# Performance work log

Hardware: AMD Instinct MI355X
Metric: run time of the kernel (lower is better)

Reference implementation:

```python
import jax, jax.numpy as jnp
import numpy as np
from jax import lax

R_WIN = 1
WIN = 2 * R_WIN + 1        # 3
K = WIN * WIN              # 9
STRIDE = 4
LATENT = 128
N_LVL = 2


def _conv_relu(x, w, b):
    # x: (B*S, 3, H, W), w: (128, 3, 7, 7) -> (B*S, 128, H/4, W/4)
    y = lax.conv_general_dilated(x, w, (STRIDE, STRIDE), [(3, 3), (3, 3)],
                                 dimension_numbers=('NCHW', 'OIHW', 'NCHW'))
    return jax.nn.relu(y + b[None, :, None, None])


def _bilinear_sample(fmap, gx, gy):
    # fmap (B,C,H,W); gx,gy (B,P) in [-1,1]; align_corners=True, zeros padding
    B, C, H, W = fmap.shape
    ix = (gx + 1.0) * 0.5 * (W - 1)
    iy = (gy + 1.0) * 0.5 * (H - 1)
    x0 = jnp.floor(ix); y0 = jnp.floor(iy)
    x1 = x0 + 1.0;      y1 = y0 + 1.0
    wx1 = ix - x0; wx0 = 1.0 - wx1
    wy1 = iy - y0; wy0 = 1.0 - wy1

    fm_flat = fmap.reshape(B, C, H * W)

    def corner(xf, yf, wgt):
        valid = (xf >= 0) & (xf <= W - 1) & (yf >= 0) & (yf <= H - 1)
        xi = jnp.clip(xf, 0, W - 1).astype(jnp.int32)
        yi = jnp.clip(yf, 0, H - 1).astype(jnp.int32)
        idx = yi * W + xi                              # (B,P)
        g = jax.vmap(lambda fm, ii: fm[:, ii])(fm_flat, idx)  # (B,C,P)
        return g * (wgt * valid)[:, None, :]

    return (corner(x0, y0, wx0 * wy0) + corner(x1, y0, wx1 * wy0)
            + corner(x0, y1, wx0 * wy1) + corner(x1, y1, wx1 * wy1))


def _sample_features(fmap, pts):
    B, C, H, W = fmap.shape
    N = pts.shape[1]
    lin = jnp.linspace(-R_WIN, R_WIN, WIN)
    dy, dx = jnp.meshgrid(lin, lin, indexing='ij')
    off = jnp.stack([dx / (W - 1) * 2.0, dy / (H - 1) * 2.0], -1).reshape(-1, 2)  # (K,2)
    grid = (pts * 2.0 - 1.0)[:, :, None, :] + off[None, None]   # (B,N,K,2)
    grid = grid.reshape(B, N * K, 2)
    s = _bilinear_sample(fmap, grid[..., 0], grid[..., 1])       # (B,C,N*K)
    return s.reshape(B, C, N, WIN, WIN)


def _l2norm(x, axis):
    return x / jnp.maximum(jnp.linalg.norm(x, axis=axis, keepdims=True), 1e-12)


def _forward(queries, frames, conv_w, conv_b, w1, b1, wp, bp, wv, bv):
    B, S, C, H, W = frames.shape
    N = queries.shape[1]
    x = 2.0 * (frames / 255.0) - 1.0
    fm = _conv_relu(x.reshape(B * S, C, H, W), conv_w, conv_b)
    fm = fm.reshape(B, S, LATENT, H // STRIDE, W // STRIDE)

    pyr = [fm]
    for _ in range(N_LVL - 1):
        fm = lax.reduce_window(fm, 0.0, lax.add, (1, 1, 1, WIN, WIN),
                               (1, 1, 1, WIN, WIN), 'VALID') / float(WIN * WIN)
        pyr.append(fm)

    cur = queries                                   # pred_pos aliases queries in torch
    vis_acc = jnp.zeros((B, N), queries.dtype)
    for i in range(N_LVL):
        f5 = pyr[N_LVL - 1 - i]                     # (B,S,C,h,w) coarse -> fine
        feats = _sample_features(f5[:, 0], cur).reshape(B, LATENT, N, K)
        matches = _sample_features(f5[:, 1], cur).reshape(B, LATENT, N, K)
        fn = _l2norm(feats, 1)
        mn = _l2norm(matches, 1)
        corr = jnp.einsum('bcnh,bcnk->bnhk', fn, mn).reshape(B * N, K * K)
        h = jax.nn.relu(corr @ w1 + b1)
        pred = jax.nn.softmax(h @ wp + bp, axis=-1).reshape(B, N, WIN, WIN)
        vis = jax.nn.sigmoid(h @ wv + bv).reshape(B, N)
        hh, ww = f5.shape[3], f5.shape[4]
        dsx = jnp.linspace(-R_WIN / (ww - 1), R_WIN / (ww - 1), WIN)
        dsy = jnp.linspace(-R_WIN / (hh - 1), R_WIN / (hh - 1), WIN)
        d_x = pred.sum(-1) @ dsx                    # (B,N)
        d_y = pred.sum(-2) @ dsy                    # (B,N)
        cur = jnp.stack([cur[..., 0] + d_x, cur[..., 1] + d_y], -1)
        vis_acc = vis_acc + vis
    return cur, vis_acc / float(N_LVL)


def setup_inputs() -> dict:
    key = jax.random.key(0)
    ks = jax.random.split(key, 8)
    B, S, N, H, W = 2, 2, 8192, 384, 512
    return {
        'queries': jax.random.uniform(ks[0], (B, N, 2), jnp.float32),
        'frames': jax.random.uniform(ks[1], (B, S, 3, H, W), jnp.float32) * 255.0,
        'conv_w': jax.random.normal(ks[2], (128, 3, 7, 7), jnp.float32) * 0.02,
        'conv_b': jnp.zeros((128,), jnp.float32),
        'w1': jax.random.normal(ks[3], (81, 256), jnp.float32) * 0.05,
        'b1': jnp.zeros((256,), jnp.float32),
        'wp': jax.random.normal(ks[4], (256, 9), jnp.float32) * 0.05,
        'bp': jnp.zeros((9,), jnp.float32),
        'wv': jax.random.normal(ks[5], (256, 1), jnp.float32) * 0.05,
        'bv': jnp.zeros((1,), jnp.float32),
    }


def reference(queries, frames, conv_w, conv_b, w1, b1, wp, bp, wv, bv):
    return _forward(queries, frames, conv_w, conv_b, w1, b1, wp, bp, wv, bv)
```

## Files before the change

### kernel.cpp

```cpp
#include <hip/hip_runtime.h>
#include <math.h>

#define NQ 8192
#define NP 16384
#define H_IN 384
#define W_IN 512
#define HH0 96
#define WW0 128
#define HH1 32
#define WW1 42

__global__ void transpose_w_kernel(const float* __restrict__ w, float* __restrict__ wT) {
    int idx = blockIdx.x * 256 + threadIdx.x;
    if (idx < 147 * 128) {
        int tap = idx >> 7;
        int oc  = idx & 127;
        wT[idx] = w[oc * 147 + tap];
    }
}

__global__ __launch_bounds__(256) void conv_kernel(
    const float* __restrict__ frames, const float* __restrict__ wT,
    const float* __restrict__ bias, float* __restrict__ out)
{
    __shared__ float lds[3 * 7 * 136];
    const int bs  = blockIdx.z;
    const int oh  = blockIdx.y;
    const int ow0 = blockIdx.x * 32;
    const int tid = threadIdx.x;

    for (int idx = tid; idx < 3 * 7 * 134; idx += 256) {
        int c   = idx / 938;
        int rem = idx - c * 938;
        int kh  = rem / 134;
        int col = rem - kh * 134;
        int gy  = oh * 4 - 3 + kh;
        int gx  = ow0 * 4 - 3 + col;
        float v = 0.0f;
        if (gy >= 0 && gy < H_IN && gx >= 0 && gx < W_IN) {
            float t = frames[((size_t)(bs * 3 + c) * H_IN + gy) * W_IN + gx];
            v = 2.0f * (t / 255.0f) - 1.0f;
        }
        lds[(c * 7 + kh) * 136 + col] = v;
    }
    __syncthreads();

    const int oc = tid & 63;
    const int g  = tid >> 6;
    float a0[8], a1[8];
#pragma unroll
    for (int p = 0; p < 8; ++p) { a0[p] = 0.0f; a1[p] = 0.0f; }

#pragma unroll
    for (int c = 0; c < 3; ++c) {
#pragma unroll
        for (int kh = 0; kh < 7; ++kh) {
            const float* row = lds + (c * 7 + kh) * 136 + g * 32;
            float4 r4[9];
#pragma unroll
            for (int j = 0; j < 9; ++j) r4[j] = *(const float4*)(row + j * 4);
            float w0[7], w1v[7];
#pragma unroll
            for (int kw = 0; kw < 7; ++kw) {
                int tap = (c * 7 + kh) * 7 + kw;
                w0[kw]  = wT[tap * 128 + oc];
                w1v[kw] = wT[tap * 128 + oc + 64];
            }
#pragma unroll
            for (int p = 0; p < 8; ++p) {
                const float4 A  = r4[p];
                const float4 Bv = r4[p + 1];
                float s0 = a0[p], s1 = a1[p];
                s0 = fmaf(A.x,  w0[0], s0);  s1 = fmaf(A.x,  w1v[0], s1);
                s0 = fmaf(A.y,  w0[1], s0);  s1 = fmaf(A.y,  w1v[1], s1);
                s0 = fmaf(A.z,  w0[2], s0);  s1 = fmaf(A.z,  w1v[2], s1);
                s0 = fmaf(A.w,  w0[3], s0);  s1 = fmaf(A.w,  w1v[3], s1);
                s0 = fmaf(Bv.x, w0[4], s0);  s1 = fmaf(Bv.x, w1v[4], s1);
                s0 = fmaf(Bv.y, w0[5], s0);  s1 = fmaf(Bv.y, w1v[5], s1);
                s0 = fmaf(Bv.z, w0[6], s0);  s1 = fmaf(Bv.z, w1v[6], s1);
                a0[p] = s0; a1[p] = s1;
            }
        }
    }

    const float b0  = bias[oc];
    const float b1b = bias[oc + 64];
#pragma unroll
    for (int p = 0; p < 8; ++p) {
        int ow = ow0 + g * 8 + p;
        size_t ob = ((size_t)(bs * HH0 + oh) * WW0 + ow) * 128;
        out[ob + oc]      = fmaxf(a0[p] + b0, 0.0f);
        out[ob + oc + 64] = fmaxf(a1[p] + b1b, 0.0f);
    }
}

__global__ void pool_kernel(const float* __restrict__ in, float* __restrict__ out) {
    int idx = blockIdx.x * 256 + threadIdx.x;
    if (idx >= 4 * HH1 * WW1 * 128) return;
    int c = idx & 127;
    int r = idx >> 7;
    int px = r % WW1; r /= WW1;
    int py = r % HH1;
    int bs = r / HH1;
    float s = 0.0f;
#pragma unroll
    for (int dy = 0; dy < 3; ++dy)
#pragma unroll
        for (int dx = 0; dx < 3; ++dx)
            s += in[(((size_t)bs * HH0 + py * 3 + dy) * WW0 + px * 3 + dx) * 128 + c];
    out[idx] = s / 9.0f;
}

__global__ __launch_bounds__(512) void sample_kernel(
    const float* __restrict__ fm, int hh, int ww,
    const float* __restrict__ cur_in, float* __restrict__ corr_out)
{
    __shared__ float smem[4 * 2400];
    const int tid  = threadIdx.x;
    const int wvi  = tid >> 6;
    const int lane = tid & 63;
    const int ps   = wvi >> 1;
    const int mp   = wvi & 1;
    const int p    = blockIdx.x * 4 + ps;
    const int b    = p >> 13;

    float* fl    = smem + ps * 2400;
    float* ml    = fl + 1188;
    float* inv_s = fl + 2376;

    const float2 pxy = *(const float2*)(cur_in + (size_t)p * 2);
    const float wwm1 = (float)(ww - 1);
    const float hhm1 = (float)(hh - 1);
    const float ix = ((pxy.x * 2.0f - 1.0f) + 1.0f) * 0.5f * wwm1;
    const float iy = ((pxy.y * 2.0f - 1.0f) + 1.0f) * 0.5f * hhm1;
    const float x0 = floorf(ix), y0 = floorf(iy);
    const float fx1 = ix - x0, fx0 = 1.0f - fx1;
    const float fy1 = iy - y0, fy0 = 1.0f - fy1;

    int   cx[4], cy[4];
    float vx[4], vy[4];
#pragma unroll
    for (int j = 0; j < 4; ++j) {
        float xc = x0 + (float)(j - 1);
        vx[j] = (xc >= 0.0f && xc <= wwm1) ? 1.0f : 0.0f;
        cx[j] = (int)fminf(fmaxf(xc, 0.0f), wwm1);
        float yc = y0 + (float)(j - 1);
        vy[j] = (yc >= 0.0f && yc <= hhm1) ? 1.0f : 0.0f;
        cy[j] = (int)fminf(fmaxf(yc, 0.0f), hhm1);
    }
    float cwx[6], cwy[6];
#pragma unroll
    for (int t = 0; t < 3; ++t) {
        cwx[t * 2 + 0] = fx0 * vx[t]; cwx[t * 2 + 1] = fx1 * vx[t + 1];
        cwy[t * 2 + 0] = fy0 * vy[t]; cwy[t * 2 + 1] = fy1 * vy[t + 1];
    }

    {
        const float2* src = (const float2*)fm + (size_t)(b * 2 + mp) * hh * ww * 64;
        float* dst = mp ? ml : fl;
        float2 P[4][4];
#pragma unroll
        for (int j = 0; j < 4; ++j)
#pragma unroll
            for (int i = 0; i < 4; ++i)
                P[j][i] = src[(cy[j] * ww + cx[i]) * 64 + lane];
#pragma unroll
        for (int ky = 0; ky < 3; ++ky)
#pragma unroll
            for (int kx = 0; kx < 3; ++kx) {
                float wA = cwy[ky * 2 + 0] * cwx[kx * 2 + 0];
                float wB = cwy[ky * 2 + 0] * cwx[kx * 2 + 1];
                float wC = cwy[ky * 2 + 1] * cwx[kx * 2 + 0];
                float wD = cwy[ky * 2 + 1] * cwx[kx * 2 + 1];
                float sx = wA * P[ky][kx].x;
                sx = fmaf(wB, P[ky][kx + 1].x, sx);
                sx = fmaf(wC, P[ky + 1][kx].x, sx);
                sx = fmaf(wD, P[ky + 1][kx + 1].x, sx);
                float sy = wA * P[ky][kx].y;
                sy = fmaf(wB, P[ky][kx + 1].y, sy);
                sy = fmaf(wC, P[ky + 1][kx].y, sy);
                sy = fmaf(wD, P[ky + 1][kx + 1].y, sy);
                *(float2*)(dst + (ky * 3 + kx) * 132 + 2 * lane) = make_float2(sx, sy);
            }
    }
    __syncthreads();

    const int e = mp * 64 + lane;
    float s = 0.0f;
    {
        const float *rA, *rB;
        if (e < 81)      { rA = fl + (e / 9) * 132; rB = ml + (e % 9) * 132; }
        else if (e < 90) { rA = fl + (e - 81) * 132; rB = rA; }
        else             { int em = e - 90; if (em > 8) em = 8;
                           rA = ml + em * 132; rB = rA; }
#pragma unroll
        for (int c = 0; c < 128; c += 4) {
            float4 a  = *(const float4*)(rA + c);
            float4 bb = *(const float4*)(rB + c);
            s += a.x * bb.x; s += a.y * bb.y; s += a.z * bb.z; s += a.w * bb.w;
        }
    }
    if (e >= 81 && e < 90)      inv_s[e - 81]     = 1.0f / fmaxf(sqrtf(s), 1e-12f);
    else if (e >= 90 && e < 99) inv_s[e - 90 + 9] = 1.0f / fmaxf(sqrtf(s), 1e-12f);
    __syncthreads();

    if (e < 81)
        corr_out[(size_t)p * 81 + e] = s * inv_s[e / 9] * inv_s[9 + e % 9];
}

__global__ __launch_bounds__(256) void mlp_kernel(
    const float* __restrict__ corr, const float* __restrict__ cur_in,
    const float* __restrict__ w1, const float* __restrict__ b1,
    const float* __restrict__ wp, const float* __restrict__ bp,
    const float* __restrict__ wvw, const float* __restrict__ bvv,
    int hh, int ww,
    float* __restrict__ cur_out,
    const float* __restrict__ vis_in, float* __restrict__ vis_out,
    int is_last)
{
    __shared__ float cls_t[81 * 18];
    __shared__ float wps[256 * 9];
    __shared__ float wvs[256];
    const int tid   = threadIdx.x;
    const int jg    = tid & 31;
    const int pg    = tid >> 5;
    const int pbase = blockIdx.x * 16;

    for (int idx = tid; idx < 16 * 81; idx += 256) {
        int pt = idx / 81, i = idx - pt * 81;
        cls_t[i * 18 + pt] = corr[(size_t)pbase * 81 + idx];
    }
    for (int idx = tid; idx < 2304; idx += 256) wps[idx] = wp[idx];
    wvs[tid] = wvw[tid];
    __syncthreads();

    float h0[8], h1[8];
    {
        const float4* bp4 = (const float4*)(b1 + jg * 8);
        float4 ba = bp4[0], bb = bp4[1];
        h0[0] = ba.x; h0[1] = ba.y; h0[2] = ba.z; h0[3] = ba.w;
        h0[4] = bb.x; h0[5] = bb.y; h0[6] = bb.z; h0[7] = bb.w;
#pragma unroll
        for (int j = 0; j < 8; ++j) h1[j] = h0[j];
    }

    const float* wbase = w1 + jg * 8;
    const float* cvbase = cls_t + pg * 2;
    for (int i = 0; i < 81; i += 3) {
        const float4 a0 = *(const float4*)(wbase + (i    ) * 256);
        const float4 a1 = *(const float4*)(wbase + (i    ) * 256 + 4);
        const float4 b0 = *(const float4*)(wbase + (i + 1) * 256);
        const float4 b1q = *(const float4*)(wbase + (i + 1) * 256 + 4);
        const float4 c0 = *(const float4*)(wbase + (i + 2) * 256);
        const float4 c1 = *(const float4*)(wbase + (i + 2) * 256 + 4);
        const float2 cvA = *(const float2*)(cvbase + (i    ) * 18);
        const float2 cvB = *(const float2*)(cvbase + (i + 1) * 18);
        const float2 cvC = *(const float2*)(cvbase + (i + 2) * 18);
        h0[0] = fmaf(cvA.x, a0.x, h0[0]); h1[0] = fmaf(cvA.y, a0.x, h1[0]);
        h0[1] = fmaf(cvA.x, a0.y, h0[1]); h1[1] = fmaf(cvA.y, a0.y, h1[1]);
        h0[2] = fmaf(cvA.x, a0.z, h0[2]); h1[2] = fmaf(cvA.y, a0.z, h1[2]);
        h0[3] = fmaf(cvA.x, a0.w, h0[3]); h1[3] = fmaf(cvA.y, a0.w, h1[3]);
        h0[4] = fmaf(cvA.x, a1.x, h0[4]); h1[4] = fmaf(cvA.y, a1.x, h1[4]);
        h0[5] = fmaf(cvA.x, a1.y, h0[5]); h1[5] = fmaf(cvA.y, a1.y, h1[5]);
        h0[6] = fmaf(cvA.x, a1.z, h0[6]); h1[6] = fmaf(cvA.y, a1.z, h1[6]);
        h0[7] = fmaf(cvA.x, a1.w, h0[7]); h1[7] = fmaf(cvA.y, a1.w, h1[7]);
        h0[0] = fmaf(cvB.x, b0.x, h0[0]); h1[0] = fmaf(cvB.y, b0.x, h1[0]);
        h0[1] = fmaf(cvB.x, b0.y, h0[1]); h1[1] = fmaf(cvB.y, b0.y, h1[1]);
        h0[2] = fmaf(cvB.x, b0.z, h0[2]); h1[2] = fmaf(cvB.y, b0.z, h1[2]);
        h0[3] = fmaf(cvB.x, b0.w, h0[3]); h1[3] = fmaf(cvB.y, b0.w, h1[3]);
        h0[4] = fmaf(cvB.x, b1q.x, h0[4]); h1[4] = fmaf(cvB.y, b1q.x, h1[4]);
        h0[5] = fmaf(cvB.x, b1q.y, h0[5]); h1[5] = fmaf(cvB.y, b1q.y, h1[5]);
        h0[6] = fmaf(cvB.x, b1q.z, h0[6]); h1[6] = fmaf(cvB.y, b1q.z, h1[6]);
        h0[7] = fmaf(cvB.x, b1q.w, h0[7]); h1[7] = fmaf(cvB.y, b1q.w, h1[7]);
        h0[0] = fmaf(cvC.x, c0.x, h0[0]); h1[0] = fmaf(cvC.y, c0.x, h1[0]);
        h0[1] = fmaf(cvC.x, c0.y, h0[1]); h1[1] = fmaf(cvC.y, c0.y, h1[1]);
        h0[2] = fmaf(cvC.x, c0.z, h0[2]); h1[2] = fmaf(cvC.y, c0.z, h1[2]);
        h0[3] = fmaf(cvC.x, c0.w, h0[3]); h1[3] = fmaf(cvC.y, c0.w, h1[3]);
        h0[4] = fmaf(cvC.x, c1.x, h0[4]); h1[4] = fmaf(cvC.y, c1.x, h1[4]);
        h0[5] = fmaf(cvC.x, c1.y, h0[5]); h1[5] = fmaf(cvC.y, c1.y, h1[5]);
        h0[6] = fmaf(cvC.x, c1.z, h0[6]); h1[6] = fmaf(cvC.y, c1.z, h1[6]);
        h0[7] = fmaf(cvC.x, c1.w, h0[7]); h1[7] = fmaf(cvC.y, c1.w, h1[7]);
    }

    float pl0[10], pl1[10];
#pragma unroll
    for (int o = 0; o < 10; ++o) { pl0[o] = 0.0f; pl1[o] = 0.0f; }
#pragma unroll
    for (int j = 0; j < 8; ++j) {
        const float hv0 = fmaxf(h0[j], 0.0f);
        const float hv1 = fmaxf(h1[j], 0.0f);
        const float* wr = wps + (jg * 8 + j) * 9;
#pragma unroll
        for (int o = 0; o < 9; ++o) {
            const float wv = wr[o];
            pl0[o] = fmaf(hv0, wv, pl0[o]);
            pl1[o] = fmaf(hv1, wv, pl1[o]);
        }
        const float wvv = wvs[jg * 8 + j];
        pl0[9] = fmaf(hv0, wvv, pl0[9]);
        pl1[9] = fmaf(hv1, wvv, pl1[9]);
    }
#pragma unroll
    for (int o = 0; o < 10; ++o) {
        pl0[o] += __shfl_xor(pl0[o], 1);  pl1[o] += __shfl_xor(pl1[o], 1);
        pl0[o] += __shfl_xor(pl0[o], 2);  pl1[o] += __shfl_xor(pl1[o], 2);
        pl0[o] += __shfl_xor(pl0[o], 4);  pl1[o] += __shfl_xor(pl1[o], 4);
        pl0[o] += __shfl_xor(pl0[o], 8);  pl1[o] += __shfl_xor(pl1[o], 8);
        pl0[o] += __shfl_xor(pl0[o], 16); pl1[o] += __shfl_xor(pl1[o], 16);
    }

    if (jg == 0) {
        const float wwm1 = (float)(ww - 1);
        const float hhm1 = (float)(hh - 1);
        const float ax = 1.0f / wwm1;
        const float ay = 1.0f / hhm1;
#pragma unroll
        for (int t = 0; t < 2; ++t) {
            const float* fo = t ? pl1 : pl0;
            const int p = pbase + pg * 2 + t;
            float lg[9];
#pragma unroll
            for (int o = 0; o < 9; ++o) lg[o] = fo[o] + bp[o];
            float mx = lg[0];
#pragma unroll
            for (int o = 1; o < 9; ++o) mx = fmaxf(mx, lg[o]);
            float ex[9], sum = 0.0f;
#pragma unroll
            for (int o = 0; o < 9; ++o) { ex[o] = expf(lg[o] - mx); sum += ex[o]; }
#pragma unroll
            for (int o = 0; o < 9; ++o) ex[o] = ex[o] / sum;

            const float vis = 1.0f / (1.0f + expf(-(fo[9] + bvv[0])));

            const float r0 = ex[0] + ex[1] + ex[2];
            const float r2 = ex[6] + ex[7] + ex[8];
            const float c0 = ex[0] + ex[3] + ex[6];
            const float c2 = ex[2] + ex[5] + ex[8];
            const float dx = r0 * (-ax) + r2 * ax;
            const float dy = c0 * (-ay) + c2 * ay;

            const float2 pq = *(const float2*)(cur_in + (size_t)p * 2);
            *(float2*)(cur_out + (size_t)p * 2) = make_float2(pq.x + dx, pq.y + dy);
            vis_out[p] = is_last ? (vis_in[p] + vis) * 0.5f : vis;
        }
    }
}

extern "C" void kernel_launch(void* const* d_in, const int* in_sizes, int n_in,
                              void* d_out, int out_size, void* d_ws, size_t ws_size,
                              hipStream_t stream) {
    (void)in_sizes; (void)n_in; (void)out_size; (void)ws_size;
    const float* queries = (const float*)d_in[0];
    const float* frames  = (const float*)d_in[1];
    const float* conv_w  = (const float*)d_in[2];
    const float* conv_b  = (const float*)d_in[3];
    const float* w1      = (const float*)d_in[4];
    const float* b1      = (const float*)d_in[5];
    const float* wp      = (const float*)d_in[6];
    const float* bp      = (const float*)d_in[7];
    const float* wvw     = (const float*)d_in[8];
    const float* bvv     = (const float*)d_in[9];
    float* out = (float*)d_out;

    float* ws     = (float*)d_ws;
    float* fm0    = ws;
    float* fm1    = fm0 + 6291456;
    float* wT     = fm1 + 688128;
    float* cur_ws = wT + 18816;
    float* vis_ws = cur_ws + 32768;
    float* corrws = vis_ws + 16384;

    transpose_w_kernel<<<74, 256, 0, stream>>>(conv_w, wT);
    conv_kernel<<<dim3(4, HH0, 4), 256, 0, stream>>>(frames, wT, conv_b, fm0);
    pool_kernel<<<2688, 256, 0, stream>>>(fm0, fm1);

    sample_kernel<<<4096, 512, 0, stream>>>(fm1, HH1, WW1, queries, corrws);
    mlp_kernel<<<1024, 256, 0, stream>>>(corrws, queries, w1, b1, wp, bp, wvw, bvv,
                                         HH1, WW1, cur_ws, nullptr, vis_ws, 0);
    sample_kernel<<<4096, 512, 0, stream>>>(fm0, HH0, WW0, cur_ws, corrws);
    mlp_kernel<<<1024, 256, 0, stream>>>(corrws, cur_ws, w1, b1, wp, bp, wvw, bvv,
                                         HH0, WW0, out, vis_ws, out + 32768, 1);
}
```

Before: 247.0 us.

## Stage MLP weights in LDS and process 64 points per block

The MLP kernel now copies the full 81x256 first-layer weight matrix into shared memory and processes 64 points per 512-thread block, with each thread computing 4 points instead of 2. This reuses each weight load across more points and replaces repeated global weight reads with LDS reads. In exchange it uses about 111KB of LDS per block, which limits occupancy, and launches only 256 blocks. The conv kernel also gets a launch-bounds occupancy hint of 4 blocks per multiprocessor, which may increase register pressure or spilling.

Result: faster. 231.7 us (-6.2%).

```diff
diff --git a/kernel.cpp b/kernel.cpp
--- a/kernel.cpp
+++ b/kernel.cpp
@@ -19,7 +19,7 @@
     }
 }
 
-__global__ __launch_bounds__(256) void conv_kernel(
+__global__ __launch_bounds__(256, 4) void conv_kernel(
     const float* __restrict__ frames, const float* __restrict__ wT,
     const float* __restrict__ bias, float* __restrict__ out)
 {
@@ -208,7 +208,7 @@
         corr_out[(size_t)p * 81 + e] = s * inv_s[e / 9] * inv_s[9 + e % 9];
 }
 
-__global__ __launch_bounds__(256) void mlp_kernel(
+__global__ __launch_bounds__(512) void mlp_kernel(
     const float* __restrict__ corr, const float* __restrict__ cur_in,
     const float* __restrict__ w1, const float* __restrict__ b1,
     const float* __restrict__ wp, const float* __restrict__ bp,
@@ -218,96 +218,86 @@
     const float* __restrict__ vis_in, float* __restrict__ vis_out,
     int is_last)
 {
-    __shared__ float cls_t[81 * 18];
-    __shared__ float wps[256 * 9];
-    __shared__ float wvs[256];
+    __shared__ float w1L[81 * 256];
+    __shared__ float corrL[81 * 68];
+    __shared__ float wpL[256 * 9];
+    __shared__ float wvL[256];
+    __shared__ float b1L[256];
     const int tid   = threadIdx.x;
     const int jg    = tid & 31;
     const int pg    = tid >> 5;
-    const int pbase = blockIdx.x * 16;
-
-    for (int idx = tid; idx < 16 * 81; idx += 256) {
+    const int j0    = jg * 8;
+    const int pbase = blockIdx.x * 64;
+
+    {
+        const float4* src = (const float4*)w1;
+        float4*       dst = (float4*)w1L;
+        for (int idx = tid; idx < 5184; idx += 512) dst[idx] = src[idx];
+    }
+    for (int idx = tid; idx < 64 * 81; idx += 512) {
         int pt = idx / 81, i = idx - pt * 81;
-        cls_t[i * 18 + pt] = corr[(size_t)pbase * 81 + idx];
-    }
-    for (int idx = tid; idx < 2304; idx += 256) wps[idx] = wp[idx];
-    wvs[tid] = wvw[tid];
+        corrL[i * 68 + pt] = corr[(size_t)pbase * 81 + idx];
+    }
+    for (int idx = tid; idx < 2304; idx += 512) wpL[idx] = wp[idx];
+    if (tid < 256) { wvL[tid] = wvw[tid]; b1L[tid] = b1[tid]; }
     __syncthreads();
 
-    float h0[8], h1[8];
-    {
-        const float4* bp4 = (const float4*)(b1 + jg * 8);
-        float4 ba = bp4[0], bb = bp4[1];
-        h0[0] = ba.x; h0[1] = ba.y; h0[2] = ba.z; h0[3] = ba.w;
-        h0[4] = bb.x; h0[5] = bb.y; h0[6] = bb.z; h0[7] = bb.w;
-#pragma unroll
-        for (int j = 0; j < 8; ++j) h1[j] = h0[j];
-    }
-
-    const float* wbase = w1 + jg * 8;
-    const float* cvbase = cls_t + pg * 2;
-    for (int i = 0; i < 81; i += 3) {
-        const float4 a0 = *(const float4*)(wbase + (i    ) * 256);
-        const float4 a1 = *(const float4*)(wbase + (i    ) * 256 + 4);
-        const float4 b0 = *(const float4*)(wbase + (i + 1) * 256);
-        const float4 b1q = *(const float4*)(wbase + (i + 1) * 256 + 4);
-        const float4 c0 = *(const float4*)(wbase + (i + 2) * 256);
-        const float4 c1 = *(const float4*)(wbase + (i + 2) * 256 + 4);
-        const float2 cvA = *(const float2*)(cvbase + (i    ) * 18);
-        const float2 cvB = *(const float2*)(cvbase + (i + 1) * 18);
-        const float2 cvC = *(const float2*)(cvbase + (i + 2) * 18);
-        h0[0] = fmaf(cvA.x, a0.x, h0[0]); h1[0] = fmaf(cvA.y, a0.x, h1[0]);
-        h0[1] = fmaf(cvA.x, a0.y, h0[1]); h1[1] = fmaf(cvA.y, a0.y, h1[1]);
-        h0[2] = fmaf(cvA.x, a0.z, h0[2]); h1[2] = fmaf(cvA.y, a0.z, h1[2]);
-        h0[3] = fmaf(cvA.x, a0.w, h0[3]); h1[3] = fmaf(cvA.y, a0.w, h1[3]);
-        h0[4] = fmaf(cvA.x, a1.x, h0[4]); h1[4] = fmaf(cvA.y, a1.x, h1[4]);
-        h0[5] = fmaf(cvA.x, a1.y, h0[5]); h1[5] = fmaf(cvA.y, a1.y, h1[5]);
-        h0[6] = fmaf(cvA.x, a1.z, h0[6]); h1[6] = fmaf(cvA.y, a1.z, h1[6]);
-        h0[7] = fmaf(cvA.x, a1.w, h0[7]); h1[7] = fmaf(cvA.y, a1.w, h1[7]);
-        h0[0] = fmaf(cvB.x, b0.x, h0[0]); h1[0] = fmaf(cvB.y, b0.x, h1[0]);
-        h0[1] = fmaf(cvB.x, b0.y, h0[1]); h1[1] = fmaf(cvB.y, b0.y, h1[1]);
-        h0[2] = fmaf(cvB.x, b0.z, h0[2]); h1[2] = fmaf(cvB.y, b0.z, h1[2]);
-        h0[3] = fmaf(cvB.x, b0.w, h0[3]); h1[3] = fmaf(cvB.y, b0.w, h1[3]);
-        h0[4] = fmaf(cvB.x, b1q.x, h0[4]); h1[4] = fmaf(cvB.y, b1q.x, h1[4]);
-        h0[5] = fmaf(cvB.x, b1q.y, h0[5]); h1[5] = fmaf(cvB.y, b1q.y, h1[5]);
-        h0[6] = fmaf(cvB.x, b1q.z, h0[6]); h1[6] = fmaf(cvB.y, b1q.z, h1[6]);
-        h0[7] = fmaf(cvB.x, b1q.w, h0[7]); h1[7] = fmaf(cvB.y, b1q.w, h1[7]);
-        h0[0] = fmaf(cvC.x, c0.x, h0[0]); h1[0] = fmaf(cvC.y, c0.x, h1[0]);
-        h0[1] = fmaf(cvC.x, c0.y, h0[1]); h1[1] = fmaf(cvC.y, c0.y, h1[1]);
-        h0[2] = fmaf(cvC.x, c0.z, h0[2]); h1[2] = fmaf(cvC.y, c0.z, h1[2]);
-        h0[3] = fmaf(cvC.x, c0.w, h0[3]); h1[3] = fmaf(cvC.y, c0.w, h1[3]);
-        h0[4] = fmaf(cvC.x, c1.x, h0[4]); h1[4] = fmaf(cvC.y, c1.x, h1[4]);
-        h0[5] = fmaf(cvC.x, c1.y, h0[5]); h1[5] = fmaf(cvC.y, c1.y, h1[5]);
-        h0[6] = fmaf(cvC.x, c1.z, h0[6]); h1[6] = fmaf(cvC.y, c1.z, h1[6]);
-        h0[7] = fmaf(cvC.x, c1.w, h0[7]); h1[7] = fmaf(cvC.y, c1.w, h1[7]);
-    }
-
-    float pl0[10], pl1[10];
-#pragma unroll
-    for (int o = 0; o < 10; ++o) { pl0[o] = 0.0f; pl1[o] = 0.0f; }
+    float h[4][8];
 #pragma unroll
     for (int j = 0; j < 8; ++j) {
-        const float hv0 = fmaxf(h0[j], 0.0f);
-        const float hv1 = fmaxf(h1[j], 0.0f);
-        const float* wr = wps + (jg * 8 + j) * 9;
-#pragma unroll
-        for (int o = 0; o < 9; ++o) {
-            const float wv = wr[o];
-            pl0[o] = fmaf(hv0, wv, pl0[o]);
-            pl1[o] = fmaf(hv1, wv, pl1[o]);
-        }
-        const float wvv = wvs[jg * 8 + j];
-        pl0[9] = fmaf(hv0, wvv, pl0[9]);
-        pl1[9] = fmaf(hv1, wvv, pl1[9]);
-    }
-#pragma unroll
-    for (int o = 0; o < 10; ++o) {
-        pl0[o] += __shfl_xor(pl0[o], 1);  pl1[o] += __shfl_xor(pl1[o], 1);
-        pl0[o] += __shfl_xor(pl0[o], 2);  pl1[o] += __shfl_xor(pl1[o], 2);
-        pl0[o] += __shfl_xor(pl0[o], 4);  pl1[o] += __shfl_xor(pl1[o], 4);
-        pl0[o] += __shfl_xor(pl0[o], 8);  pl1[o] += __shfl_xor(pl1[o], 8);
-        pl0[o] += __shfl_xor(pl0[o], 16); pl1[o] += __shfl_xor(pl1[o], 16);
-    }
+        const float bj = b1L[j0 + j];
+#pragma unroll
+        for (int p = 0; p < 4; ++p) h[p][j] = bj;
+    }
+
+    const float* wlp = w1L + j0;
+    const float* cvp = corrL + pg * 4;
+#pragma unroll 3
+    for (int i = 0; i < 81; ++i) {
+        const float4 wa = *(const float4*)(wlp + i * 256);
+        const float4 wb = *(const float4*)(wlp + i * 256 + 4);
+        const float4 cv = *(const float4*)(cvp + i * 68);
+        const float c4[4] = {cv.x, cv.y, cv.z, cv.w};
+#pragma unroll
+        for (int p = 0; p < 4; ++p) {
+            h[p][0] = fmaf(c4[p], wa.x, h[p][0]);
+            h[p][1] = fmaf(c4[p], wa.y, h[p][1]);
+            h[p][2] = fmaf(c4[p], wa.z, h[p][2]);
+            h[p][3] = fmaf(c4[p], wa.w, h[p][3]);
+            h[p][4] = fmaf(c4[p], wb.x, h[p][4]);
+            h[p][5] = fmaf(c4[p], wb.y, h[p][5]);
+            h[p][6] = fmaf(c4[p], wb.z, h[p][6]);
+            h[p][7] = fmaf(c4[p], wb.w, h[p][7]);
+        }
+    }
+
+    float pl[4][10];
+#pragma unroll
+    for (int p = 0; p < 4; ++p)
+#pragma unroll
+        for (int o = 0; o < 10; ++o) pl[p][o] = 0.0f;
+#pragma unroll
+    for (int j = 0; j < 8; ++j) {
+        const float* wr = wpL + (j0 + j) * 9;
+        const float wvv = wvL[j0 + j];
+#pragma unroll
+        for (int p = 0; p < 4; ++p) {
+            const float hv = fmaxf(h[p][j], 0.0f);
+#pragma unroll
+            for (int o = 0; o < 9; ++o) pl[p][o] = fmaf(hv, wr[o], pl[p][o]);
+            pl[p][9] = fmaf(hv, wvv, pl[p][9]);
+        }
+    }
+#pragma unroll
+    for (int p = 0; p < 4; ++p)
+#pragma unroll
+        for (int o = 0; o < 10; ++o) {
+            pl[p][o] += __shfl_xor(pl[p][o], 1);
+            pl[p][o] += __shfl_xor(pl[p][o], 2);
+            pl[p][o] += __shfl_xor(pl[p][o], 4);
+            pl[p][o] += __shfl_xor(pl[p][o], 8);
+            pl[p][o] += __shfl_xor(pl[p][o], 16);
+        }
 
     if (jg == 0) {
         const float wwm1 = (float)(ww - 1);
@@ -315,9 +305,9 @@
         const float ax = 1.0f / wwm1;
         const float ay = 1.0f / hhm1;
 #pragma unroll
-        for (int t = 0; t < 2; ++t) {
-            const float* fo = t ? pl1 : pl0;
-            const int p = pbase + pg * 2 + t;
+        for (int t = 0; t < 4; ++t) {
+            const float* fo = pl[t];
+            const int p = pbase + pg * 4 + t;
             float lg[9];
 #pragma unroll
             for (int o = 0; o < 9; ++o) lg[o] = fo[o] + bp[o];
@@ -375,9 +365,9 @@
     pool_kernel<<<2688, 256, 0, stream>>>(fm0, fm1);
 
     sample_kernel<<<4096, 512, 0, stream>>>(fm1, HH1, WW1, queries, corrws);
-    mlp_kernel<<<1024, 256, 0, stream>>>(corrws, queries, w1, b1, wp, bp, wvw, bvv,
-                                         HH1, WW1, cur_ws, nullptr, vis_ws, 0);
+    mlp_kernel<<<256, 512, 0, stream>>>(corrws, queries, w1, b1, wp, bp, wvw, bvv,
+                                        HH1, WW1, cur_ws, nullptr, vis_ws, 0);
     sample_kernel<<<4096, 512, 0, stream>>>(fm0, HH0, WW0, cur_ws, corrws);
-    mlp_kernel<<<1024, 256, 0, stream>>>(corrws, cur_ws, w1, b1, wp, bp, wvw, bvv,
-                                         HH0, WW0, out, vis_ws, out + 32768, 1);
-}
+    mlp_kernel<<<256, 512, 0, stream>>>(corrws, cur_ws, w1, b1, wp, bp, wvw, bvv,
+                                        HH0, WW0, out, vis_ws, out + 32768, 1);
+}
```
